# Kernel optimization log

Measured on AMD Instinct MI355X. Metric: run time of the kernel, lower is better.

Reference implementation:

```python
import jax, jax.numpy as jnp
import numpy as np

OWN_DIM = 7
INTR_DIM = 5
N_HEADS = 3
HEAD_DIM = 5
N_INTR = 256
BATCH = 32768
H1, H2 = 256, 256
ACTION_DIM = 2
IN_DIM = OWN_DIM + N_HEADS * HEAD_DIM  # 22
SCALE = np.sqrt(HEAD_DIM).astype(np.float32)
LN_EPS = 1e-5


def setup_inputs() -> dict:
    key = jax.random.key(0)
    ks = jax.random.split(key, 16)
    f32 = jnp.float32
    inp = {
        "obs": jax.random.normal(ks[0], (BATCH, OWN_DIM + N_INTR * INTR_DIM), dtype=f32),
        "Wq": jax.random.normal(ks[1], (N_HEADS, OWN_DIM, HEAD_DIM), dtype=f32) * 0.4,
        "bq": jnp.zeros((N_HEADS, HEAD_DIM), dtype=f32),
        "Wk": jax.random.normal(ks[2], (N_HEADS, INTR_DIM, HEAD_DIM), dtype=f32) * 0.4,
        "bk": jnp.zeros((N_HEADS, HEAD_DIM), dtype=f32),
        "Wv": jax.random.normal(ks[3], (N_HEADS, INTR_DIM, HEAD_DIM), dtype=f32) * 0.4,
        "bv": jnp.zeros((N_HEADS, HEAD_DIM), dtype=f32),
        "v_att": jax.random.normal(ks[4], (N_HEADS, HEAD_DIM), dtype=f32) * 0.5,
        "temperature": jnp.ones((1,), dtype=f32) * 3.0,
        "ln_g": jnp.ones((IN_DIM,), dtype=f32),
        "ln_b": jnp.zeros((IN_DIM,), dtype=f32),
        "W1": jax.random.normal(ks[5], (IN_DIM, H1), dtype=f32) * 0.15,
        "b1": jnp.zeros((H1,), dtype=f32),
        "W2": jax.random.normal(ks[6], (H1, H2), dtype=f32) * 0.08,
        "b2": jnp.zeros((H2,), dtype=f32),
        "Wf": jax.random.normal(ks[7], (H2, ACTION_DIM), dtype=f32) * 0.08,
        "bf": jnp.zeros((ACTION_DIM,), dtype=f32),
        "log_std": jnp.zeros((ACTION_DIM,), dtype=f32),
    }
    return inp


def reference(obs, Wq, bq, Wk, bk, Wv, bv, v_att, temperature,
              ln_g, ln_b, W1, b1, W2, b2, Wf, bf, log_std):
    own = obs[:, :OWN_DIM]                                   # [B, 7]
    intr = obs[:, OWN_DIM:OWN_DIM + N_INTR * INTR_DIM]
    intr = intr.reshape(-1, N_INTR, INTR_DIM)                # [B, N, 5]

    # all heads at once
    q = jnp.einsum("bo,hod->bhd", own, Wq) + bq              # [B, H, D]
    k = jnp.einsum("bni,hid->bhnd", intr, Wk) + bk[None, :, None, :]
    v = jnp.einsum("bni,hid->bhnd", intr, Wv) + bv[None, :, None, :]

    energy = jnp.tanh(q[:, :, None, :] + k)                  # [B, H, N, D]
    scores = jnp.einsum("bhnd,hd->bhn", energy, v_att)
    scores = scores / SCALE * jnp.abs(temperature[0])

    is_padding = jnp.sum(jnp.abs(intr), axis=2) < 1e-6       # [B, N]
    scores = jnp.where(is_padding[:, None, :], -jnp.inf, scores)
    alpha = jax.nn.softmax(scores, axis=-1)
    alpha = jnp.nan_to_num(alpha, nan=0.0)                   # all-padded rows -> 0

    context = jnp.einsum("bhn,bhnd->bhd", alpha, v)          # [B, H, D]
    context = context.reshape(context.shape[0], N_HEADS * HEAD_DIM)

    x = jnp.concatenate([own, context], axis=1)              # [B, 22]
    mu = jnp.mean(x, axis=-1, keepdims=True)
    var = jnp.mean(jnp.square(x - mu), axis=-1, keepdims=True)
    x = (x - mu) * jax.lax.rsqrt(var + LN_EPS) * ln_g + ln_b

    x = jax.nn.leaky_relu(x @ W1 + b1, negative_slope=0.2)
    x = jax.nn.leaky_relu(x @ W2 + b2, negative_slope=0.2)
    out = x @ Wf + bf                                        # [B, 2]

    log_std_exp = jnp.broadcast_to(log_std[None, :], (out.shape[0], ACTION_DIM))
    return jnp.concatenate([out, log_std_exp], axis=1)       # [B, 4]
```

## Files before the change

### kernel.cpp

```cpp
#include <hip/hip_runtime.h>
#include <math.h>

#define NBATCH   32768
#define OWN_DIM  7
#define INTR_DIM 5
#define N_HEADS  3
#define HEAD_DIM 5
#define N_INTR   256
#define ROWLEN   1287
#define XDIM     22
#define H1DIM    256
#define H2DIM    256

typedef __attribute__((ext_vector_type(8))) short bf16x8;
typedef __attribute__((ext_vector_type(4))) float f32x4;

__device__ __forceinline__ float leaky02(float x) {
    return fmaxf(x, 0.2f * x);
}

__device__ __forceinline__ unsigned short f2bf_rne(float f) {
    unsigned u = __float_as_uint(f);
    return (unsigned short)((u + 0x7FFFu + ((u >> 16) & 1u)) >> 16);
}

__global__ __launch_bounds__(256, 4) void attn_ln_kernel(
    const float* __restrict__ obs,
    const float* __restrict__ Wq, const float* __restrict__ bq,
    const float* __restrict__ Wk, const float* __restrict__ bk,
    const float* __restrict__ Wv, const float* __restrict__ bv,
    const float* __restrict__ v_att, const float* __restrict__ temp,
    const float* __restrict__ ln_g, const float* __restrict__ ln_b,
    float* __restrict__ xout)
{
    const int wid  = threadIdx.x >> 6;
    const int lane = threadIdx.x & 63;
    const int grp  = lane >> 4;
    const int gl   = lane & 15;
    const int s    = blockIdx.x * 16 + wid * 4 + grp;
    const float* row = obs + (size_t)s * ROWLEN;

    const float fac = fabsf(temp[0]) * 0.4472135954999579f;
    const float facl2e = fac * 1.4426950408889634f;
    const float TL2E = 2.885390081777927f;

    float own[OWN_DIM];
    #pragma unroll
    for (int o = 0; o < OWN_DIM; ++o) own[o] = row[o];

    float va2[N_HEADS][HEAD_DIM], vasum[N_HEADS];
    #pragma unroll
    for (int h = 0; h < N_HEADS; ++h) {
        float ssum = 0.0f;
        #pragma unroll
        for (int d = 0; d < HEAD_DIM; ++d) {
            float v = v_att[h*HEAD_DIM + d];
            ssum += v;
            va2[h][d] = v * (-2.0f * facl2e);
        }
        vasum[h] = ssum * facl2e;
    }

    float qb[N_HEADS][HEAD_DIM];
    #pragma unroll
    for (int h = 0; h < N_HEADS; ++h)
        #pragma unroll
        for (int d = 0; d < HEAD_DIM; ++d) {
            float a = bq[h*HEAD_DIM + d] + bk[h*HEAD_DIM + d];
            #pragma unroll
            for (int o = 0; o < OWN_DIM; ++o)
                a = fmaf(own[o], Wq[h*OWN_DIM*HEAD_DIM + o*HEAD_DIM + d], a);
            qb[h][d] = a;
        }

    float svp[N_HEADS][INTR_DIM] = {};
    float es[N_HEADS] = {};

    #pragma unroll
    for (int r = 0; r < 16; ++r) {
        const float* it = row + OWN_DIM + (gl + 16*r) * INTR_DIM;
        float xi[INTR_DIM];
        #pragma unroll
        for (int i = 0; i < INTR_DIM; ++i) xi[i] = it[i];
        float asum = fabsf(xi[0]) + fabsf(xi[1]) + fabsf(xi[2])
                   + fabsf(xi[3]) + fabsf(xi[4]);
        const float npf = (asum < 1e-6f) ? 0.0f : 1.0f;
        #pragma unroll
        for (int h = 0; h < N_HEADS; ++h) {
            float dot = vasum[h];
            #pragma unroll
            for (int d = 0; d < HEAD_DIM; ++d) {
                float t = qb[h][d];
                #pragma unroll
                for (int i = 0; i < INTR_DIM; ++i)
                    t = fmaf(xi[i], Wk[h*INTR_DIM*HEAD_DIM + i*HEAD_DIM + d], t);
                float e = __builtin_amdgcn_exp2f(t * TL2E);
                float rc = __builtin_amdgcn_rcpf(e + 1.0f);
                dot = fmaf(va2[h][d], rc, dot);
            }
            float e = npf * __builtin_amdgcn_exp2f(dot);
            es[h] += e;
            #pragma unroll
            for (int i = 0; i < INTR_DIM; ++i)
                svp[h][i] = fmaf(e, xi[i], svp[h][i]);
        }
    }

    #pragma unroll
    for (int o = 1; o < 16; o <<= 1) {
        #pragma unroll
        for (int h = 0; h < N_HEADS; ++h) {
            es[h] += __shfl_xor(es[h], o, 64);
            #pragma unroll
            for (int i = 0; i < INTR_DIM; ++i)
                svp[h][i] += __shfl_xor(svp[h][i], o, 64);
        }
    }

    float ctx[N_HEADS][HEAD_DIM];
    #pragma unroll
    for (int h = 0; h < N_HEADS; ++h) {
        const float live = (es[h] > 0.0f) ? 1.0f : 0.0f;
        const float rinv = live * __builtin_amdgcn_rcpf(es[h]);
        float svn[INTR_DIM];
        #pragma unroll
        for (int i = 0; i < INTR_DIM; ++i) svn[i] = svp[h][i] * rinv;
        #pragma unroll
        for (int d = 0; d < HEAD_DIM; ++d) {
            float c = bv[h*HEAD_DIM + d] * live;
            #pragma unroll
            for (int i = 0; i < INTR_DIM; ++i)
                c = fmaf(svn[i], Wv[h*INTR_DIM*HEAD_DIM + i*HEAD_DIM + d], c);
            ctx[h][d] = c;
        }
    }

    float sum = 0.0f;
    #pragma unroll
    for (int o = 0; o < OWN_DIM; ++o) sum += own[o];
    #pragma unroll
    for (int h = 0; h < N_HEADS; ++h)
        #pragma unroll
        for (int d = 0; d < HEAD_DIM; ++d) sum += ctx[h][d];
    const float mu = sum * (1.0f / 22.0f);
    float var = 0.0f;
    #pragma unroll
    for (int o = 0; o < OWN_DIM; ++o) { float dd = own[o] - mu; var += dd*dd; }
    #pragma unroll
    for (int h = 0; h < N_HEADS; ++h)
        #pragma unroll
        for (int d = 0; d < HEAD_DIM; ++d) { float dd = ctx[h][d] - mu; var += dd*dd; }
    var *= (1.0f / 22.0f);
    const float rs = rsqrtf(var + 1e-5f);

    float xv0 = own[0];
    #pragma unroll
    for (int o = 1; o < OWN_DIM; ++o) xv0 = (gl == o) ? own[o] : xv0;
    #pragma unroll
    for (int j = 0; j < 15; ++j) xv0 = (gl == OWN_DIM + j) ? ctx[j/5][j%5] : xv0;
    float xv1 = ctx[1][4];
    #pragma unroll
    for (int j = 10; j < 15; ++j) xv1 = (gl == j - 9) ? ctx[j/5][j%5] : xv1;

    float* xo = xout + (size_t)s * XDIM;
    xo[gl] = (xv0 - mu) * rs * ln_g[gl] + ln_b[gl];
    if (gl < XDIM - 16) {
        xo[16 + gl] = (xv1 - mu) * rs * ln_g[16 + gl] + ln_b[16 + gl];
    }
}

__global__ __launch_bounds__(256) void mlp_kernel(
    const float* __restrict__ x,
    const float* __restrict__ W1, const float* __restrict__ b1,
    const float* __restrict__ W2, const float* __restrict__ b2,
    const float* __restrict__ Wf, const float* __restrict__ bf,
    const float* __restrict__ lstd, float* __restrict__ out)
{
    __shared__ __align__(16) float xs[32 * XDIM];
    __shared__ __align__(16) unsigned char h1b[32 * 256 * 2];
    __shared__ __align__(16) unsigned char w2b[256 * 64 * 2];
    __shared__ __align__(16) float wfs[H2DIM * 2];
    __shared__ float oacc[4][32][2];

    const int t   = threadIdx.x;
    const int blk = blockIdx.x;

    for (int i = t; i < 32 * XDIM; i += 256) xs[i] = x[(size_t)blk * 32 * XDIM + i];
    for (int i = t; i < H2DIM * 2; i += 256) wfs[i] = Wf[i];

    float w1r[XDIM];
    #pragma unroll
    for (int i = 0; i < XDIM; ++i) w1r[i] = W1[i * H1DIM + t];
    const float b1t = b1[t];
    __syncthreads();
    for (int e = 0; e < 32; ++e) {
        float a = b1t;
        #pragma unroll
        for (int i = 0; i < XDIM; ++i) a += xs[e * XDIM + i] * w1r[i];
        a = leaky02(a);
        int byte = e * 512 + t * 2;
        byte ^= ((e & 7) << 4);
        *(unsigned short*)(h1b + byte) = f2bf_rne(a);
    }

    const int wv_  = t >> 6;
    const int lane = t & 63;
    const int mrow = lane & 15;
    const int qk   = lane >> 4;

    f32x4 acc[2][4];
    #pragma unroll
    for (int mt = 0; mt < 2; ++mt)
        #pragma unroll
        for (int nt = 0; nt < 4; ++nt)
            acc[mt][nt] = (f32x4){0.f, 0.f, 0.f, 0.f};

    for (int kc = 0; kc < 4; ++kc) {
        __syncthreads();
        {
            const int n = t;
            #pragma unroll
            for (int k8 = 0; k8 < 64; k8 += 8) {
                bf16x8 v;
                #pragma unroll
                for (int j = 0; j < 8; ++j) {
                    float w = W2[(size_t)(kc * 64 + k8 + j) * H2DIM + n];
                    v[j] = (short)f2bf_rne(w);
                }
                int byte = n * 128 + k8 * 2;
                byte ^= ((n & 7) << 4);
                *(bf16x8*)(w2b + byte) = v;
            }
        }
        __syncthreads();
        #pragma unroll
        for (int ks = 0; ks < 2; ++ks) {
            const int klocal = ks * 32;
            const int kglob  = kc * 64 + klocal;
            bf16x8 afrag[2], bfrag[4];
            #pragma unroll
            for (int mt = 0; mt < 2; ++mt) {
                const int rowi = mt * 16 + mrow;
                int byte = rowi * 512 + (kglob + 8 * qk) * 2;
                byte ^= ((rowi & 7) << 4);
                afrag[mt] = *(const bf16x8*)(h1b + byte);
            }
            #pragma unroll
            for (int nt = 0; nt < 4; ++nt) {
                const int col = wv_ * 64 + nt * 16 + mrow;
                int byte = col * 128 + (klocal + 8 * qk) * 2;
                byte ^= ((col & 7) << 4);
                bfrag[nt] = *(const bf16x8*)(w2b + byte);
            }
            #pragma unroll
            for (int mt = 0; mt < 2; ++mt)
                #pragma unroll
                for (int nt = 0; nt < 4; ++nt)
                    acc[mt][nt] = __builtin_amdgcn_mfma_f32_16x16x32_bf16(
                        afrag[mt], bfrag[nt], acc[mt][nt], 0, 0, 0);
        }
    }

    float b2n[4];
    #pragma unroll
    for (int nt = 0; nt < 4; ++nt) b2n[nt] = b2[wv_ * 64 + nt * 16 + mrow];

    float p[8][2];
    #pragma unroll
    for (int i = 0; i < 8; ++i) { p[i][0] = 0.f; p[i][1] = 0.f; }
    #pragma unroll
    for (int mt = 0; mt < 2; ++mt)
        #pragma unroll
        for (int nt = 0; nt < 4; ++nt) {
            const int n = wv_ * 64 + nt * 16 + mrow;
            #pragma unroll
            for (int reg = 0; reg < 4; ++reg) {
                float h2v = leaky02(acc[mt][nt][reg] + b2n[nt]);
                p[mt*4 + reg][0] = fmaf(h2v, wfs[2*n + 0], p[mt*4 + reg][0]);
                p[mt*4 + reg][1] = fmaf(h2v, wfs[2*n + 1], p[mt*4 + reg][1]);
            }
        }
    #pragma unroll
    for (int o = 1; o < 16; o <<= 1) {
        #pragma unroll
        for (int i = 0; i < 8; ++i) {
            p[i][0] += __shfl_xor(p[i][0], o, 64);
            p[i][1] += __shfl_xor(p[i][1], o, 64);
        }
    }
    if (mrow == 0) {
        #pragma unroll
        for (int mt = 0; mt < 2; ++mt)
            #pragma unroll
            for (int reg = 0; reg < 4; ++reg) {
                const int sample = mt * 16 + qk * 4 + reg;
                oacc[wv_][sample][0] = p[mt*4 + reg][0];
                oacc[wv_][sample][1] = p[mt*4 + reg][1];
            }
    }
    __syncthreads();
    if (t < 32) {
        float o0 = bf[0], o1 = bf[1];
        #pragma unroll
        for (int w = 0; w < 4; ++w) { o0 += oacc[w][t][0]; o1 += oacc[w][t][1]; }
        float4 o4;
        o4.x = o0; o4.y = o1; o4.z = lstd[0]; o4.w = lstd[1];
        *(float4*)&out[(size_t)(blk * 32 + t) * 4] = o4;
    }
}

extern "C" void kernel_launch(void* const* d_in, const int* in_sizes, int n_in,
                              void* d_out, int out_size, void* d_ws, size_t ws_size,
                              hipStream_t stream) {
    const float* obs   = (const float*)d_in[0];
    const float* Wq    = (const float*)d_in[1];
    const float* bq    = (const float*)d_in[2];
    const float* Wk    = (const float*)d_in[3];
    const float* bk    = (const float*)d_in[4];
    const float* Wv    = (const float*)d_in[5];
    const float* bv    = (const float*)d_in[6];
    const float* v_att = (const float*)d_in[7];
    const float* temp  = (const float*)d_in[8];
    const float* ln_g  = (const float*)d_in[9];
    const float* ln_b  = (const float*)d_in[10];
    const float* W1    = (const float*)d_in[11];
    const float* b1    = (const float*)d_in[12];
    const float* W2    = (const float*)d_in[13];
    const float* b2    = (const float*)d_in[14];
    const float* Wf    = (const float*)d_in[15];
    const float* bf    = (const float*)d_in[16];
    const float* lstd  = (const float*)d_in[17];

    float* xbuf = (float*)d_ws;
    float* outf = (float*)d_out;

    attn_ln_kernel<<<NBATCH / 16, 256, 0, stream>>>(
        obs, Wq, bq, Wk, bk, Wv, bv, v_att, temp, ln_g, ln_b, xbuf);
    mlp_kernel<<<NBATCH / 32, 256, 0, stream>>>(
        xbuf, W1, b1, W2, b2, Wf, bf, lstd, outf);
}
```

Baseline: 91.61 us.

## Stage observation rows through LDS with coalesced loads and register prefetch

Each 16-lane group now loads its obs row in contiguous 336-float chunks using coalesced dword loads and writes them into a per-group LDS window. The attention loop then reads the 5 interaction features per item from LDS instead of strided global memory. The next chunk is prefetched into registers while the current one is processed, so global latency overlaps with the tanh/exp math. The cost is extra LDS traffic, about 21 more live registers per thread that may reduce occupancy, and possible LDS bank conflicts from the stride-5 reads.

New measurement: 122.0 us. +33.2%, slower.

```diff
diff --git a/kernel.cpp b/kernel.cpp
--- a/kernel.cpp
+++ b/kernel.cpp
@@ -12,6 +12,9 @@
 #define H1DIM    256
 #define H2DIM    256
 
+#define WCHUNK   336
+#define NJ       21
+
 typedef __attribute__((ext_vector_type(8))) short bf16x8;
 typedef __attribute__((ext_vector_type(4))) float f32x4;
 
@@ -33,12 +36,14 @@
     const float* __restrict__ ln_g, const float* __restrict__ ln_b,
     float* __restrict__ xout)
 {
+    __shared__ float smem[4][4][WCHUNK];
     const int wid  = threadIdx.x >> 6;
     const int lane = threadIdx.x & 63;
     const int grp  = lane >> 4;
     const int gl   = lane & 15;
     const int s    = blockIdx.x * 16 + wid * 4 + grp;
     const float* row = obs + (size_t)s * ROWLEN;
+    float* win = smem[wid][grp];
 
     const float fac = fabsf(temp[0]) * 0.4472135954999579f;
     const float facl2e = fac * 1.4426950408889634f;
@@ -76,33 +81,57 @@
     float svp[N_HEADS][INTR_DIM] = {};
     float es[N_HEADS] = {};
 
-    #pragma unroll
-    for (int r = 0; r < 16; ++r) {
-        const float* it = row + OWN_DIM + (gl + 16*r) * INTR_DIM;
-        float xi[INTR_DIM];
-        #pragma unroll
-        for (int i = 0; i < INTR_DIM; ++i) xi[i] = it[i];
-        float asum = fabsf(xi[0]) + fabsf(xi[1]) + fabsf(xi[2])
-                   + fabsf(xi[3]) + fabsf(xi[4]);
-        const float npf = (asum < 1e-6f) ? 0.0f : 1.0f;
-        #pragma unroll
-        for (int h = 0; h < N_HEADS; ++h) {
-            float dot = vasum[h];
-            #pragma unroll
-            for (int d = 0; d < HEAD_DIM; ++d) {
-                float t = qb[h][d];
+    float cur[NJ];
+    #pragma unroll
+    for (int j = 0; j < NJ; ++j) cur[j] = row[j*16 + gl];
+
+    #pragma unroll
+    for (int c = 0; c < 4; ++c) {
+        #pragma unroll
+        for (int j = 0; j < NJ; ++j) win[j*16 + gl] = cur[j];
+
+        float nxt[NJ];
+        if (c < 3) {
+            #pragma unroll
+            for (int j = 0; j < NJ; ++j) {
+                const int idx = (c + 1) * 320 + j*16 + gl;
+                nxt[j] = (idx < ROWLEN) ? row[idx] : 0.0f;
+            }
+        }
+
+        #pragma unroll
+        for (int rr = 0; rr < 4; ++rr) {
+            const int off = 7 + (gl + 16*rr) * INTR_DIM;
+            float xi[INTR_DIM];
+            #pragma unroll
+            for (int i = 0; i < INTR_DIM; ++i) xi[i] = win[off + i];
+            float asum = fabsf(xi[0]) + fabsf(xi[1]) + fabsf(xi[2])
+                       + fabsf(xi[3]) + fabsf(xi[4]);
+            const float npf = (asum < 1e-6f) ? 0.0f : 1.0f;
+            #pragma unroll
+            for (int h = 0; h < N_HEADS; ++h) {
+                float dot = vasum[h];
+                #pragma unroll
+                for (int d = 0; d < HEAD_DIM; ++d) {
+                    float t = qb[h][d];
+                    #pragma unroll
+                    for (int i = 0; i < INTR_DIM; ++i)
+                        t = fmaf(xi[i], Wk[h*INTR_DIM*HEAD_DIM + i*HEAD_DIM + d], t);
+                    float e = __builtin_amdgcn_exp2f(t * TL2E);
+                    float rc = __builtin_amdgcn_rcpf(e + 1.0f);
+                    dot = fmaf(va2[h][d], rc, dot);
+                }
+                float e = npf * __builtin_amdgcn_exp2f(dot);
+                es[h] += e;
                 #pragma unroll
                 for (int i = 0; i < INTR_DIM; ++i)
-                    t = fmaf(xi[i], Wk[h*INTR_DIM*HEAD_DIM + i*HEAD_DIM + d], t);
-                float e = __builtin_amdgcn_exp2f(t * TL2E);
-                float rc = __builtin_amdgcn_rcpf(e + 1.0f);
-                dot = fmaf(va2[h][d], rc, dot);
-            }
-            float e = npf * __builtin_amdgcn_exp2f(dot);
-            es[h] += e;
-            #pragma unroll
-            for (int i = 0; i < INTR_DIM; ++i)
-                svp[h][i] = fmaf(e, xi[i], svp[h][i]);
+                    svp[h][i] = fmaf(e, xi[i], svp[h][i]);
+            }
+        }
+
+        if (c < 3) {
+            #pragma unroll
+            for (int j = 0; j < NJ; ++j) cur[j] = nxt[j];
         }
     }
 
```

## Stage interaction rows through LDS with direct global-to-LDS loads

Applied to the files above, without the earlier changes.

Replaces the strided per-lane global loads of interaction features (5 floats at stride 5 per lane) with coalesced global_load_lds copies of each warp's four rows into shared memory, in four chunks of 320 floats. Threads then read their features from LDS. The goal is fully coalesced DRAM traffic instead of scattered 4-byte accesses. In exchange it adds explicit waits between chunks that serialize load and compute, and uses 24KB of shared memory per block, which may limit occupancy.

Result: slower. 148.9 us (+62.5%).

```diff
diff --git a/kernel.cpp b/kernel.cpp
--- a/kernel.cpp
+++ b/kernel.cpp
@@ -12,6 +12,8 @@
 #define H1DIM    256
 #define H2DIM    256
 
+#define WDW      384
+
 typedef __attribute__((ext_vector_type(8))) short bf16x8;
 typedef __attribute__((ext_vector_type(4))) float f32x4;
 
@@ -22,6 +24,12 @@
 __device__ __forceinline__ unsigned short f2bf_rne(float f) {
     unsigned u = __float_as_uint(f);
     return (unsigned short)((u + 0x7FFFu + ((u >> 16) & 1u)) >> 16);
+}
+
+__device__ __forceinline__ void gload_lds4(const float* g, float* l) {
+    __builtin_amdgcn_global_load_lds(
+        (const __attribute__((address_space(1))) void*)g,
+        (__attribute__((address_space(3)))  void*)l, 4, 0, 0);
 }
 
 __global__ __launch_bounds__(256, 4) void attn_ln_kernel(
@@ -33,12 +41,14 @@
     const float* __restrict__ ln_g, const float* __restrict__ ln_b,
     float* __restrict__ xout)
 {
+    __shared__ float smem[4][4][WDW];
     const int wid  = threadIdx.x >> 6;
     const int lane = threadIdx.x & 63;
     const int grp  = lane >> 4;
     const int gl   = lane & 15;
     const int s    = blockIdx.x * 16 + wid * 4 + grp;
-    const float* row = obs + (size_t)s * ROWLEN;
+    const float* row  = obs + (size_t)s * ROWLEN;
+    const float* wrow = obs + (size_t)(blockIdx.x * 16 + wid * 4) * ROWLEN;
 
     const float fac = fabsf(temp[0]) * 0.4472135954999579f;
     const float facl2e = fac * 1.4426950408889634f;
@@ -77,32 +87,53 @@
     float es[N_HEADS] = {};
 
     #pragma unroll
-    for (int r = 0; r < 16; ++r) {
-        const float* it = row + OWN_DIM + (gl + 16*r) * INTR_DIM;
-        float xi[INTR_DIM];
-        #pragma unroll
-        for (int i = 0; i < INTR_DIM; ++i) xi[i] = it[i];
-        float asum = fabsf(xi[0]) + fabsf(xi[1]) + fabsf(xi[2])
-                   + fabsf(xi[3]) + fabsf(xi[4]);
-        const float npf = (asum < 1e-6f) ? 0.0f : 1.0f;
-        #pragma unroll
-        for (int h = 0; h < N_HEADS; ++h) {
-            float dot = vasum[h];
-            #pragma unroll
-            for (int d = 0; d < HEAD_DIM; ++d) {
-                float t = qb[h][d];
+    for (int c = 0; c < 4; ++c) {
+        if (c > 0) {
+            asm volatile("s_waitcnt lgkmcnt(0)" ::: "memory");
+            __builtin_amdgcn_sched_barrier(0);
+        }
+        #pragma unroll
+        for (int r = 0; r < 4; ++r) {
+            const float* rbase = wrow + (size_t)r * ROWLEN + c * 320;
+            #pragma unroll
+            for (int j = 0; j < 6; ++j) {
+                int idx = j * 64 + lane;
+                if (c == 3 && j == 5) idx = (idx > 326) ? 326 : idx;
+                gload_lds4(rbase + idx, &smem[wid][r][j * 64]);
+            }
+        }
+        asm volatile("s_waitcnt vmcnt(0)" ::: "memory");
+        __builtin_amdgcn_sched_barrier(0);
+
+        const float* win = smem[wid][grp];
+        #pragma unroll
+        for (int rr = 0; rr < 4; ++rr) {
+            const int off = 7 + (gl + 16 * rr) * INTR_DIM;
+            float xi[INTR_DIM];
+            #pragma unroll
+            for (int i = 0; i < INTR_DIM; ++i) xi[i] = win[off + i];
+            float asum = fabsf(xi[0]) + fabsf(xi[1]) + fabsf(xi[2])
+                       + fabsf(xi[3]) + fabsf(xi[4]);
+            const float npf = (asum < 1e-6f) ? 0.0f : 1.0f;
+            #pragma unroll
+            for (int h = 0; h < N_HEADS; ++h) {
+                float dot = vasum[h];
+                #pragma unroll
+                for (int d = 0; d < HEAD_DIM; ++d) {
+                    float t = qb[h][d];
+                    #pragma unroll
+                    for (int i = 0; i < INTR_DIM; ++i)
+                        t = fmaf(xi[i], Wk[h*INTR_DIM*HEAD_DIM + i*HEAD_DIM + d], t);
+                    float e = __builtin_amdgcn_exp2f(t * TL2E);
+                    float rc = __builtin_amdgcn_rcpf(e + 1.0f);
+                    dot = fmaf(va2[h][d], rc, dot);
+                }
+                float e = npf * __builtin_amdgcn_exp2f(dot);
+                es[h] += e;
                 #pragma unroll
                 for (int i = 0; i < INTR_DIM; ++i)
-                    t = fmaf(xi[i], Wk[h*INTR_DIM*HEAD_DIM + i*HEAD_DIM + d], t);
-                float e = __builtin_amdgcn_exp2f(t * TL2E);
-                float rc = __builtin_amdgcn_rcpf(e + 1.0f);
-                dot = fmaf(va2[h][d], rc, dot);
-            }
-            float e = npf * __builtin_amdgcn_exp2f(dot);
-            es[h] += e;
-            #pragma unroll
-            for (int i = 0; i < INTR_DIM; ++i)
-                svp[h][i] = fmaf(e, xi[i], svp[h][i]);
+                    svp[h][i] = fmaf(e, xi[i], svp[h][i]);
+            }
         }
     }
 
```

## Vectorize intruder loads with aligned float4 reads and remap samples to waves

Applied to the files above, without the earlier changes.

Each lane now handles 4 consecutive intruders (20 floats) per step and reads them with aligned 16-byte vector loads. A per-wave misalignment offset selects the extraction pattern. The sample-to-wave mapping is changed so all lanes of a wave share the same row alignment (row length 1287 mod 4), which keeps the switch wave-uniform. This is meant to cut the number of scalar global load instructions, in exchange for some over-read, more registers and a four-way code expansion.

Measured after the change: 199.3 us. 118% more time.

```diff
diff --git a/kernel.cpp b/kernel.cpp
--- a/kernel.cpp
+++ b/kernel.cpp
@@ -37,8 +37,9 @@
     const int lane = threadIdx.x & 63;
     const int grp  = lane >> 4;
     const int gl   = lane & 15;
-    const int s    = blockIdx.x * 16 + wid * 4 + grp;
+    const int s    = blockIdx.x * 16 + grp * 4 + wid;
     const float* row = obs + (size_t)s * ROWLEN;
+    const int o    = (3 * (wid + 1)) & 3;
 
     const float fac = fabsf(temp[0]) * 0.4472135954999579f;
     const float facl2e = fac * 1.4426950408889634f;
@@ -46,7 +47,7 @@
 
     float own[OWN_DIM];
     #pragma unroll
-    for (int o = 0; o < OWN_DIM; ++o) own[o] = row[o];
+    for (int oo = 0; oo < OWN_DIM; ++oo) own[oo] = row[oo];
 
     float va2[N_HEADS][HEAD_DIM], vasum[N_HEADS];
     #pragma unroll
@@ -68,52 +69,79 @@
         for (int d = 0; d < HEAD_DIM; ++d) {
             float a = bq[h*HEAD_DIM + d] + bk[h*HEAD_DIM + d];
             #pragma unroll
-            for (int o = 0; o < OWN_DIM; ++o)
-                a = fmaf(own[o], Wq[h*OWN_DIM*HEAD_DIM + o*HEAD_DIM + d], a);
+            for (int oo = 0; oo < OWN_DIM; ++oo)
+                a = fmaf(own[oo], Wq[h*OWN_DIM*HEAD_DIM + oo*HEAD_DIM + d], a);
             qb[h][d] = a;
         }
 
     float svp[N_HEADS][INTR_DIM] = {};
     float es[N_HEADS] = {};
 
-    #pragma unroll
-    for (int r = 0; r < 16; ++r) {
-        const float* it = row + OWN_DIM + (gl + 16*r) * INTR_DIM;
-        float xi[INTR_DIM];
-        #pragma unroll
-        for (int i = 0; i < INTR_DIM; ++i) xi[i] = it[i];
-        float asum = fabsf(xi[0]) + fabsf(xi[1]) + fabsf(xi[2])
-                   + fabsf(xi[3]) + fabsf(xi[4]);
-        const float npf = (asum < 1e-6f) ? 0.0f : 1.0f;
-        #pragma unroll
-        for (int h = 0; h < N_HEADS; ++h) {
-            float dot = vasum[h];
-            #pragma unroll
-            for (int d = 0; d < HEAD_DIM; ++d) {
-                float t = qb[h][d];
+    #define XI_EXTRACT(O, NV)                                             \
+        {                                                                 \
+            _Pragma("unroll")                                             \
+            for (int j = 0; j < (NV); ++j) v[j] = vp[j];                  \
+            _Pragma("unroll")                                             \
+            for (int k = 0; k < 4; ++k) {                                 \
+                _Pragma("unroll")                                         \
+                for (int i = 0; i < INTR_DIM; ++i) {                      \
+                    const int f = (O) + 5*k + i;                          \
+                    xi4[k][i] = v[f >> 2][f & 3];                         \
+                }                                                         \
+            }                                                             \
+        }
+
+    #pragma unroll
+    for (int t = 0; t < 4; ++t) {
+        const int base_f = OWN_DIM + (4 * gl + 64 * t) * INTR_DIM;
+        const f32x4* vp = (const f32x4*)(row + base_f - o);
+        float xi4[4][INTR_DIM];
+        {
+            f32x4 v[6];
+            switch (o) {
+                case 0:  XI_EXTRACT(0, 5); break;
+                case 1:  XI_EXTRACT(1, 6); break;
+                case 2:  XI_EXTRACT(2, 6); break;
+                default: XI_EXTRACT(3, 6); break;
+            }
+        }
+        #pragma unroll
+        for (int k = 0; k < 4; ++k) {
+            const float* xi = xi4[k];
+            float asum = fabsf(xi[0]) + fabsf(xi[1]) + fabsf(xi[2])
+                       + fabsf(xi[3]) + fabsf(xi[4]);
+            const float npf = (asum < 1e-6f) ? 0.0f : 1.0f;
+            #pragma unroll
+            for (int h = 0; h < N_HEADS; ++h) {
+                float dot = vasum[h];
+                #pragma unroll
+                for (int d = 0; d < HEAD_DIM; ++d) {
+                    float tq = qb[h][d];
+                    #pragma unroll
+                    for (int i = 0; i < INTR_DIM; ++i)
+                        tq = fmaf(xi[i], Wk[h*INTR_DIM*HEAD_DIM + i*HEAD_DIM + d], tq);
+                    float e = __builtin_amdgcn_exp2f(tq * TL2E);
+                    float rc = __builtin_amdgcn_rcpf(e + 1.0f);
+                    dot = fmaf(va2[h][d], rc, dot);
+                }
+                float e = npf * __builtin_amdgcn_exp2f(dot);
+                es[h] += e;
                 #pragma unroll
                 for (int i = 0; i < INTR_DIM; ++i)
-                    t = fmaf(xi[i], Wk[h*INTR_DIM*HEAD_DIM + i*HEAD_DIM + d], t);
-                float e = __builtin_amdgcn_exp2f(t * TL2E);
-                float rc = __builtin_amdgcn_rcpf(e + 1.0f);
-                dot = fmaf(va2[h][d], rc, dot);
-            }
-            float e = npf * __builtin_amdgcn_exp2f(dot);
-            es[h] += e;
+                    svp[h][i] = fmaf(e, xi[i], svp[h][i]);
+            }
+        }
+    }
+    #undef XI_EXTRACT
+
+    #pragma unroll
+    for (int off = 1; off < 16; off <<= 1) {
+        #pragma unroll
+        for (int h = 0; h < N_HEADS; ++h) {
+            es[h] += __shfl_xor(es[h], off, 64);
             #pragma unroll
             for (int i = 0; i < INTR_DIM; ++i)
-                svp[h][i] = fmaf(e, xi[i], svp[h][i]);
-        }
-    }
-
-    #pragma unroll
-    for (int o = 1; o < 16; o <<= 1) {
-        #pragma unroll
-        for (int h = 0; h < N_HEADS; ++h) {
-            es[h] += __shfl_xor(es[h], o, 64);
-            #pragma unroll
-            for (int i = 0; i < INTR_DIM; ++i)
-                svp[h][i] += __shfl_xor(svp[h][i], o, 64);
+                svp[h][i] += __shfl_xor(svp[h][i], off, 64);
         }
     }
 
@@ -137,7 +165,7 @@
 
     float sum = 0.0f;
     #pragma unroll
-    for (int o = 0; o < OWN_DIM; ++o) sum += own[o];
+    for (int oo = 0; oo < OWN_DIM; ++oo) sum += own[oo];
     #pragma unroll
     for (int h = 0; h < N_HEADS; ++h)
         #pragma unroll
@@ -145,7 +173,7 @@
     const float mu = sum * (1.0f / 22.0f);
     float var = 0.0f;
     #pragma unroll
-    for (int o = 0; o < OWN_DIM; ++o) { float dd = own[o] - mu; var += dd*dd; }
+    for (int oo = 0; oo < OWN_DIM; ++oo) { float dd = own[oo] - mu; var += dd*dd; }
     #pragma unroll
     for (int h = 0; h < N_HEADS; ++h)
         #pragma unroll
@@ -155,7 +183,7 @@
 
     float xv0 = own[0];
     #pragma unroll
-    for (int o = 1; o < OWN_DIM; ++o) xv0 = (gl == o) ? own[o] : xv0;
+    for (int oo = 1; oo < OWN_DIM; ++oo) xv0 = (gl == oo) ? own[oo] : xv0;
     #pragma unroll
     for (int j = 0; j < 15; ++j) xv0 = (gl == OWN_DIM + j) ? ctx[j/5][j%5] : xv0;
     float xv1 = ctx[1][4];
@@ -281,11 +309,11 @@
             }
         }
     #pragma unroll
-    for (int o = 1; o < 16; o <<= 1) {
+    for (int off = 1; off < 16; off <<= 1) {
         #pragma unroll
         for (int i = 0; i < 8; ++i) {
-            p[i][0] += __shfl_xor(p[i][0], o, 64);
-            p[i][1] += __shfl_xor(p[i][1], o, 64);
+            p[i][0] += __shfl_xor(p[i][0], off, 64);
+            p[i][1] += __shfl_xor(p[i][1], off, 64);
         }
     }
     if (mrow == 0) {
```
